# Performance work log

Measured on AMD Instinct MI355X. Metric: run time of the kernel, lower is better.

The kernel has to match this reference:

```python
import jax, jax.numpy as jnp
import numpy as np

B, M, D = 8, 8192, 1024   # batch, tokens, latent_dim
N, P = 128, 1             # num_experts, slots_per_expert
F = 4096                  # expert_dim


def setup_inputs() -> dict:
    key = jax.random.key(0)
    k_x, k_phi, k_w1, k_b1, k_w2, k_b2 = jax.random.split(key, 6)
    x = jax.random.normal(k_x, (B, M, D), dtype=jnp.float32)
    # phi initialized as randn(d, n, p) / sqrt(d) in the original
    phi = jax.random.normal(k_phi, (D, N, P), dtype=jnp.float32) / (D ** 0.5)
    # Single shared expert MLP (original aliases one nn.Sequential across all experts)
    W1 = jax.random.normal(k_w1, (D, F), dtype=jnp.float32) / (D ** 0.5)
    b1 = jax.random.normal(k_b1, (F,), dtype=jnp.float32) * 0.01
    W2 = jax.random.normal(k_w2, (F, D), dtype=jnp.float32) / (F ** 0.5)
    b2 = jax.random.normal(k_b2, (D,), dtype=jnp.float32) * 0.01
    return {"x": x, "phi": phi, "W1": W1, "b1": b1, "W2": W2, "b2": b2}


def reference(x, phi, W1, b1, W2, b2):
    # dispatch / combine logits: [b, m, n, p]
    logits = jnp.einsum('bmd,dnp->bmnp', x, phi)
    d = jax.nn.softmax(logits, axis=1)                      # softmax over tokens m
    b_, m_, n_, p_ = logits.shape
    c = jax.nn.softmax(logits.reshape(b_, m_, n_ * p_), axis=-1).reshape(b_, m_, n_, p_)
    # slot inputs: [b, n, p, d]
    x_i = jnp.einsum('bmd,bmnp->bnpd', x, d)
    # shared expert MLP (torch GELU default = exact erf)
    h = jax.nn.gelu(jnp.einsum('bnpd,df->bnpf', x_i, W1) + b1, approximate=False)
    y_i = jnp.einsum('bnpf,fd->bnpd', h, W2) + b2
    # combine: [b, m, d]
    y = jnp.einsum('bnpd,bmnp->bmd', y_i, c)
    return y
```

## Files before the change

### kernel.cpp

```cpp
#include <hip/hip_runtime.h>
#include <math.h>

#define Bq 8
#define Mq 8192
#define Dq 1024
#define Nq 128
#define Fq 4096

typedef __bf16 bf16x8 __attribute__((ext_vector_type(8)));
typedef float f32x4 __attribute__((ext_vector_type(4)));
union P4 { __bf16 h[4]; unsigned long long u; };
union H8 { int4 v; _Float16 h[8]; };
union B8 { int4 v; __bf16 h[8]; };

__device__ __forceinline__ int swz128(int row, int bcol) {
  return row * 128 + (bcol ^ ((row & 7) << 4));
}
__device__ __forceinline__ int swz256(int row, int bcol) {
  return row * 256 + (bcol ^ ((row & 7) << 4));
}

__global__ __launch_bounds__(256) void wconv(const float* __restrict__ src,
                                             unsigned long long* __restrict__ dst, long n4)
{
  long i = (long)blockIdx.x * 256 + threadIdx.x;
  if (i >= n4) return;
  float4 v = ((const float4*)src)[i];
  P4 p; p.h[0] = (__bf16)v.x; p.h[1] = (__bf16)v.y; p.h[2] = (__bf16)v.z; p.h[3] = (__bf16)v.w;
  dst[i] = p.u;
}

__global__ __launch_bounds__(256) void logits_mfma(
    const float* __restrict__ x, const float* __restrict__ phi,
    __bf16* __restrict__ eT, __bf16* __restrict__ cbuf)
{
  __shared__ __align__(16) char sA[16384];
  __shared__ __align__(16) char sP[16384];
  int mt = blockIdx.x, b = blockIdx.y;
  int m0 = mt * 128;
  int t = threadIdx.x;
  int col = t & 127, half = t >> 7;
  int arow = t >> 4, ac4 = t & 15;
  int w = t >> 6, l = t & 63, la = l & 15, lb = l >> 4;

  f32x4 zero = {0.f, 0.f, 0.f, 0.f};
  f32x4 acc[2][8];
  for (int i = 0; i < 2; ++i) for (int j = 0; j < 8; ++j) acc[i][j] = zero;

  for (int k0 = 0; k0 < Dq; k0 += 64) {
    #pragma unroll
    for (int i = 0; i < 8; ++i) {
      int row = arow + 16 * i;
      float4 v = *(const float4*)(x + ((long)b * Mq + m0 + row) * Dq + k0 + ac4 * 4);
      P4 p;
      p.h[0] = (__bf16)v.x; p.h[1] = (__bf16)v.y;
      p.h[2] = (__bf16)v.z; p.h[3] = (__bf16)v.w;
      *(unsigned long long*)(sA + swz128(row, 8 * ac4)) = p.u;
    }
    {
      const float* Pp = phi + (long)(k0 + half * 32) * Nq + col;
      #pragma unroll
      for (int i = 0; i < 32; i += 4) {
        float a0 = Pp[(i + 0) * Nq], a1 = Pp[(i + 1) * Nq];
        float a2 = Pp[(i + 2) * Nq], a3 = Pp[(i + 3) * Nq];
        P4 p;
        p.h[0] = (__bf16)a0; p.h[1] = (__bf16)a1;
        p.h[2] = (__bf16)a2; p.h[3] = (__bf16)a3;
        *(unsigned long long*)(sP + swz128(col, 2 * (half * 32 + i))) = p.u;
      }
    }
    __syncthreads();
    #pragma unroll
    for (int sub = 0; sub < 2; ++sub) {
      int mbyte = sub * 64 + lb * 16;
      bf16x8 af0 = *(const bf16x8*)(sA + swz128(w * 32 + la, mbyte));
      bf16x8 af1 = *(const bf16x8*)(sA + swz128(w * 32 + 16 + la, mbyte));
      bf16x8 bv[8];
      #pragma unroll
      for (int j = 0; j < 8; ++j)
        bv[j] = *(const bf16x8*)(sP + swz128(j * 16 + la, mbyte));
      #pragma unroll
      for (int j = 0; j < 8; ++j) {
        acc[0][j] = __builtin_amdgcn_mfma_f32_16x16x32_bf16(af0, bv[j], acc[0][j], 0, 0, 0);
        acc[1][j] = __builtin_amdgcn_mfma_f32_16x16x32_bf16(af1, bv[j], acc[1][j], 0, 0, 0);
      }
    }
    __syncthreads();
  }
  float inv[2][4];
  #pragma unroll
  for (int i = 0; i < 2; ++i)
    #pragma unroll
    for (int r = 0; r < 4; ++r) {
      float s = 0.f;
      #pragma unroll
      for (int j = 0; j < 8; ++j) s += __expf(acc[i][j][r]);
      s += __shfl_xor(s, 1); s += __shfl_xor(s, 2);
      s += __shfl_xor(s, 4); s += __shfl_xor(s, 8);
      inv[i][r] = 1.0f / s;
    }
  __bf16* Cb = cbuf + ((long)b * Mq + m0) * Nq;
  __bf16* Eb = eT + (long)b * Nq * Mq + m0;
  #pragma unroll
  for (int i = 0; i < 2; ++i)
    #pragma unroll
    for (int j = 0; j < 8; ++j) {
      P4 p;
      #pragma unroll
      for (int r = 0; r < 4; ++r) {
        int row = w * 32 + i * 16 + lb * 4 + r;
        float e = __expf(acc[i][j][r]);
        p.h[r] = (__bf16)e;
        Cb[(long)row * Nq + j * 16 + la] = (__bf16)(e * inv[i][r]);
      }
      *(unsigned long long*)(Eb + (long)(j * 16 + la) * Mq + w * 32 + i * 16 + lb * 4) = p.u;
    }
}

__global__ __launch_bounds__(256) void colsum_rows(const __bf16* __restrict__ eT,
                                                   float* __restrict__ cinv)
{
  __shared__ float red[4];
  int r = blockIdx.x;
  int t = threadIdx.x;
  const __bf16* p = eT + (long)r * Mq;
  float s = 0.f;
  #pragma unroll
  for (int k = 0; k < 4; ++k) {
    B8 v; v.v = *(const int4*)(p + t * 8 + k * 2048);
    #pragma unroll
    for (int e = 0; e < 8; ++e) s += (float)v.h[e];
  }
  #pragma unroll
  for (int off = 32; off >= 1; off >>= 1) s += __shfl_down(s, off);
  if ((t & 63) == 0) red[t >> 6] = s;
  __syncthreads();
  if (t == 0) cinv[r] = 1.0f / (red[0] + red[1] + red[2] + red[3]);
}

__global__ __launch_bounds__(256) void xi_mfma(
    const __bf16* __restrict__ eT, const float* __restrict__ x,
    _Float16* __restrict__ part)
{
  __shared__ __align__(16) char sD[16384];
  __shared__ __align__(16) char sX[8192];
  int dt = blockIdx.x, kc = blockIdx.y, b = blockIdx.z;
  int d0 = dt * 64;
  int t = threadIdx.x;
  int arow = t >> 1, ahalf = t & 1;
  const __bf16* Ep0 = eT + ((long)b * Nq + arow) * Mq + (long)kc * 1024 + ahalf * 32;
  int cd = t & 63, grp = t >> 6;
  const float* Xp0 = x + ((long)b * Mq + (long)kc * 1024 + grp * 16) * Dq + d0 + cd;
  int w = t >> 6, l = t & 63, la = l & 15, lb = l >> 4;

  f32x4 zero = {0.f, 0.f, 0.f, 0.f};
  f32x4 acc[2][4];
  for (int i = 0; i < 2; ++i) for (int j = 0; j < 4; ++j) acc[i][j] = zero;

  int4 ar[4];
  float br[16];
  #pragma unroll
  for (int q = 0; q < 4; ++q) ar[q] = *(const int4*)(Ep0 + q * 8);
  #pragma unroll
  for (int i = 0; i < 16; ++i) br[i] = Xp0[(long)i * Dq];
  #pragma unroll
  for (int q = 0; q < 4; ++q)
    *(int4*)(sD + swz128(arow, ahalf * 64 + q * 16)) = ar[q];
  #pragma unroll
  for (int q = 0; q < 4; ++q) {
    P4 p;
    p.h[0] = (__bf16)br[4 * q + 0]; p.h[1] = (__bf16)br[4 * q + 1];
    p.h[2] = (__bf16)br[4 * q + 2]; p.h[3] = (__bf16)br[4 * q + 3];
    *(unsigned long long*)(sX + swz128(cd, grp * 32 + q * 8)) = p.u;
  }

  for (int it = 0; it < 16; ++it) {
    __syncthreads();
    if (it < 15) {
      #pragma unroll
      for (int q = 0; q < 4; ++q)
        ar[q] = *(const int4*)(Ep0 + (it + 1) * 64 + q * 8);
      #pragma unroll
      for (int i = 0; i < 16; ++i)
        br[i] = Xp0[((long)(it + 1) * 64 + i) * Dq];
    }
    #pragma unroll
    for (int sub = 0; sub < 2; ++sub) {
      int mbyte = sub * 64 + lb * 16;
      bf16x8 af0 = *(const bf16x8*)(sD + swz128(w * 32 + la, mbyte));
      bf16x8 af1 = *(const bf16x8*)(sD + swz128(w * 32 + 16 + la, mbyte));
      bf16x8 bv[4];
      #pragma unroll
      for (int j = 0; j < 4; ++j)
        bv[j] = *(const bf16x8*)(sX + swz128(j * 16 + la, mbyte));
      #pragma unroll
      for (int j = 0; j < 4; ++j) {
        acc[0][j] = __builtin_amdgcn_mfma_f32_16x16x32_bf16(af0, bv[j], acc[0][j], 0, 0, 0);
        acc[1][j] = __builtin_amdgcn_mfma_f32_16x16x32_bf16(af1, bv[j], acc[1][j], 0, 0, 0);
      }
    }
    __syncthreads();
    if (it < 15) {
      #pragma unroll
      for (int q = 0; q < 4; ++q)
        *(int4*)(sD + swz128(arow, ahalf * 64 + q * 16)) = ar[q];
      #pragma unroll
      for (int q = 0; q < 4; ++q) {
        P4 p;
        p.h[0] = (__bf16)br[4 * q + 0]; p.h[1] = (__bf16)br[4 * q + 1];
        p.h[2] = (__bf16)br[4 * q + 2]; p.h[3] = (__bf16)br[4 * q + 3];
        *(unsigned long long*)(sX + swz128(cd, grp * 32 + q * 8)) = p.u;
      }
    }
  }
  _Float16* P = part + ((long)kc * Bq + b) * (long)Nq * Dq + d0;
  #pragma unroll
  for (int i = 0; i < 2; ++i)
    #pragma unroll
    for (int j = 0; j < 4; ++j)
      #pragma unroll
      for (int r = 0; r < 4; ++r)
        P[(long)(w * 32 + i * 16 + lb * 4 + r) * Dq + j * 16 + la] = (_Float16)acc[i][j][r];
}

__global__ __launch_bounds__(256) void xi_reduce(const _Float16* __restrict__ part,
    const float* __restrict__ cinv, __bf16* __restrict__ xib)
{
  long base = ((long)blockIdx.x * 256 + threadIdx.x) * 8;
  int row = (int)(base >> 10);
  float civ = cinv[row];
  float s[8] = {};
  #pragma unroll
  for (int k = 0; k < 8; ++k) {
    H8 v; v.v = *(const int4*)(part + (long)k * 1048576 + base);
    #pragma unroll
    for (int e = 0; e < 8; ++e) s[e] += (float)v.h[e];
  }
  B8 o;
  #pragma unroll
  for (int e = 0; e < 8; ++e) o.h[e] = (__bf16)(s[e] * civ);
  *(int4*)(xib + base) = o.v;
}

template<int EPI, typename OT>
__global__ __launch_bounds__(256) void gemm_bf16(const __bf16* __restrict__ A,
    const __bf16* __restrict__ Bw, const float* __restrict__ bias,
    OT* __restrict__ C, int lda, int ldb, int ldc, int kLen, long strideCz)
{
  __shared__ __align__(16) char sA[16384];
  __shared__ __align__(16) char sB[16384];
  int m0 = blockIdx.x * 128, n0 = blockIdx.y * 128;
  int kbase = blockIdx.z * kLen;
  C += (long)blockIdx.z * strideCz;
  int t = threadIdx.x;
  int col = t & 127, half = t >> 7;
  int w = t >> 6, l = t & 63, la = l & 15, lb = l >> 4;

  f32x4 zero = {0.f, 0.f, 0.f, 0.f};
  f32x4 acc[2][8];
  for (int i = 0; i < 2; ++i) for (int j = 0; j < 8; ++j) acc[i][j] = zero;

  for (int kt = 0; kt < kLen; kt += 64) {
    int kp = kbase + kt;
    #pragma unroll
    for (int s = 0; s < 4; ++s) {
      int idx = t + 256 * s;
      int row = idx >> 3, c8 = idx & 7;
      *(int4*)(sA + swz128(row, c8 * 16)) =
          *(const int4*)(A + (long)(m0 + row) * lda + kp + c8 * 8);
    }
    {
      const __bf16* Bp = Bw + (long)(kp + half * 32) * ldb + n0 + col;
      #pragma unroll
      for (int i = 0; i < 32; i += 4) {
        P4 p;
        p.h[0] = Bp[(long)(i + 0) * ldb]; p.h[1] = Bp[(long)(i + 1) * ldb];
        p.h[2] = Bp[(long)(i + 2) * ldb]; p.h[3] = Bp[(long)(i + 3) * ldb];
        *(unsigned long long*)(sB + swz128(col, 2 * (half * 32 + i))) = p.u;
      }
    }
    __syncthreads();
    #pragma unroll
    for (int sub = 0; sub < 2; ++sub) {
      int mbyte = sub * 64 + lb * 16;
      bf16x8 af0 = *(const bf16x8*)(sA + swz128(w * 32 + la, mbyte));
      bf16x8 af1 = *(const bf16x8*)(sA + swz128(w * 32 + 16 + la, mbyte));
      bf16x8 bv[8];
      #pragma unroll
      for (int j = 0; j < 8; ++j)
        bv[j] = *(const bf16x8*)(sB + swz128(j * 16 + la, mbyte));
      #pragma unroll
      for (int j = 0; j < 8; ++j) {
        acc[0][j] = __builtin_amdgcn_mfma_f32_16x16x32_bf16(af0, bv[j], acc[0][j], 0, 0, 0);
        acc[1][j] = __builtin_amdgcn_mfma_f32_16x16x32_bf16(af1, bv[j], acc[1][j], 0, 0, 0);
      }
    }
    __syncthreads();
  }
  #pragma unroll
  for (int i = 0; i < 2; ++i)
    #pragma unroll
    for (int j = 0; j < 8; ++j)
      #pragma unroll
      for (int r = 0; r < 4; ++r) {
        int row = m0 + w * 32 + i * 16 + lb * 4 + r;
        int colg = n0 + j * 16 + la;
        float v = acc[i][j][r];
        if (EPI == 2) {
          v += bias[colg];
          v = 0.5f * v * (1.0f + erff(v * 0.70710678118654752f));
        }
        C[(long)row * ldc + colg] = (OT)v;
      }
}

__global__ __launch_bounds__(256) void g2_reduce(const float* __restrict__ part,
    const float* __restrict__ b2, __bf16* __restrict__ yiT)
{
  long idx = (long)blockIdx.x * 256 + threadIdx.x;
  int row = (int)(idx >> 10);
  int d = (int)(idx & 1023);
  float s = part[idx] + part[idx + 1048576] + part[idx + 2097152] + part[idx + 3145728] + b2[d];
  int b = row >> 7, n = row & 127;
  yiT[((long)b * Dq + d) * Nq + n] = (__bf16)s;
}

__global__ __launch_bounds__(256) void combine_mfma(const __bf16* __restrict__ cbuf,
    const __bf16* __restrict__ yiT, float* __restrict__ y)
{
  __shared__ __align__(16) char sC[32768];
  __shared__ __align__(16) char sY[32768];
  int mt = blockIdx.x, dt = blockIdx.y, b = blockIdx.z;
  int m0 = mt * 128, d0 = dt * 128;
  int t = threadIdx.x;
  #pragma unroll
  for (int s = 0; s < 8; ++s) {
    int idx = t + 256 * s;
    int row = idx >> 4, c16 = idx & 15;
    *(int4*)(sC + swz256(row, c16 * 16)) =
        *(const int4*)(cbuf + ((long)b * Mq + m0 + row) * Nq + c16 * 8);
    *(int4*)(sY + swz256(row, c16 * 16)) =
        *(const int4*)(yiT + ((long)b * Dq + d0 + row) * Nq + c16 * 8);
  }
  __syncthreads();
  int w = t >> 6, l = t & 63, la = l & 15, lb = l >> 4;
  f32x4 zero = {0.f, 0.f, 0.f, 0.f};
  f32x4 acc[2][8];
  for (int i = 0; i < 2; ++i) for (int j = 0; j < 8; ++j) acc[i][j] = zero;
  #pragma unroll
  for (int sub = 0; sub < 4; ++sub) {
    int mbyte = sub * 64 + lb * 16;
    bf16x8 af0 = *(const bf16x8*)(sC + swz256(w * 32 + la, mbyte));
    bf16x8 af1 = *(const bf16x8*)(sC + swz256(w * 32 + 16 + la, mbyte));
    bf16x8 bv[8];
    #pragma unroll
    for (int j = 0; j < 8; ++j)
      bv[j] = *(const bf16x8*)(sY + swz256(j * 16 + la, mbyte));
    #pragma unroll
    for (int j = 0; j < 8; ++j) {
      acc[0][j] = __builtin_amdgcn_mfma_f32_16x16x32_bf16(af0, bv[j], acc[0][j], 0, 0, 0);
      acc[1][j] = __builtin_amdgcn_mfma_f32_16x16x32_bf16(af1, bv[j], acc[1][j], 0, 0, 0);
    }
  }
  float* Y = y + ((long)b * Mq + m0) * Dq + d0;
  #pragma unroll
  for (int i = 0; i < 2; ++i)
    #pragma unroll
    for (int j = 0; j < 8; ++j)
      #pragma unroll
      for (int r = 0; r < 4; ++r)
        Y[(long)(w * 32 + i * 16 + lb * 4 + r) * Dq + j * 16 + la] = acc[i][j][r];
}

extern "C" void kernel_launch(void* const* d_in, const int* in_sizes, int n_in,
                              void* d_out, int out_size, void* d_ws, size_t ws_size,
                              hipStream_t stream) {
  const float* x   = (const float*)d_in[0];
  const float* phi = (const float*)d_in[1];
  const float* W1  = (const float*)d_in[2];
  const float* b1  = (const float*)d_in[3];
  const float* W2  = (const float*)d_in[4];
  const float* b2  = (const float*)d_in[5];
  float* y = (float*)d_out;

  char* W = (char*)d_ws;
  __bf16*   cbuf   = (__bf16*)W;
  __bf16*   eT     = (__bf16*)(W + 16777216);
  __bf16*   h      = eT;
  _Float16* part   = (_Float16*)(W + 33554432);
  float*    g2part = (float*)(W + 33554432);
  __bf16*   W1b    = (__bf16*)(W + 50331648);
  __bf16*   W2b    = (__bf16*)(W + 58720256);
  __bf16*   xib    = (__bf16*)(W + 67108864);
  __bf16*   yiT    = (__bf16*)(W + 69206016);
  float*    cinv   = (float*)(W + 71303168);

  wconv<<<4096, 256, 0, stream>>>(W1, (unsigned long long*)W1b, 1048576);
  wconv<<<4096, 256, 0, stream>>>(W2, (unsigned long long*)W2b, 1048576);
  logits_mfma<<<dim3(Mq / 128, Bq), 256, 0, stream>>>(x, phi, eT, cbuf);
  colsum_rows<<<Bq * Nq, 256, 0, stream>>>(eT, cinv);
  xi_mfma<<<dim3(Dq / 64, 8, Bq), 256, 0, stream>>>(eT, x, part);
  xi_reduce<<<512, 256, 0, stream>>>(part, cinv, xib);
  gemm_bf16<2, __bf16><<<dim3(8, 32, 1), 256, 0, stream>>>(
      xib, W1b, b1, h, Dq, Fq, Fq, 1024, 0L);
  gemm_bf16<0, float><<<dim3(8, 8, 4), 256, 0, stream>>>(
      h, W2b, nullptr, g2part, Fq, Dq, Dq, 1024, 1048576L);
  g2_reduce<<<4096, 256, 0, stream>>>(g2part, b2, yiT);
  combine_mfma<<<dim3(Mq / 128, Dq / 128, Bq), 256, 0, stream>>>(cbuf, yiT, y);
}
```

Before: 440.0 us.

## Widen xi_mfma d-tile, vectorize x loads, and remap block order for L2 locality

The x_i GEMM kernel now covers 128 d-columns per block instead of 64. That halves the number of blocks re-reading the dispatch weights, and each thread loads x as float4 rows instead of scalar strided loads, at the cost of scalar bf16 transposed writes into shared memory. Both xi_mfma and combine_mfma switch to a 1D grid with a remapped block index, so neighbouring blocks share inputs and are spread across XCDs, which should improve L2 reuse. The wider tile doubles accumulator registers and grows shared memory, which may lower occupancy.

```diff
diff --git a/kernel.cpp b/kernel.cpp
--- a/kernel.cpp
+++ b/kernel.cpp
@@ -143,81 +143,73 @@
     _Float16* __restrict__ part)
 {
   __shared__ __align__(16) char sD[16384];
-  __shared__ __align__(16) char sX[8192];
-  int dt = blockIdx.x, kc = blockIdx.y, b = blockIdx.z;
-  int d0 = dt * 64;
+  __shared__ __align__(16) char sX[16384];
+  int lin = blockIdx.x;
+  int wk = (lin & 7) * 64 + (lin >> 3);
+  int dts = wk & 7, kc = (wk >> 3) & 7, b = wk >> 6;
+  int d0 = dts * 128;
   int t = threadIdx.x;
+  int w = t >> 6, l = t & 63, la = l & 15, lb = l >> 4;
   int arow = t >> 1, ahalf = t & 1;
-  const __bf16* Ep0 = eT + ((long)b * Nq + arow) * Mq + (long)kc * 1024 + ahalf * 32;
-  int cd = t & 63, grp = t >> 6;
-  const float* Xp0 = x + ((long)b * Mq + (long)kc * 1024 + grp * 16) * Dq + d0 + cd;
-  int w = t >> 6, l = t & 63, la = l & 15, lb = l >> 4;
+  const __bf16* Ep0 = eT + ((long)b * Nq + arow) * Mq + kc * 1024 + ahalf * 32;
+  int bm = w * 2 + (l >> 5), bd = (l & 31) * 4;
+  const float* Xp0 = x + ((long)b * Mq + kc * 1024 + bm) * Dq + d0 + bd;
 
   f32x4 zero = {0.f, 0.f, 0.f, 0.f};
-  f32x4 acc[2][4];
-  for (int i = 0; i < 2; ++i) for (int j = 0; j < 4; ++j) acc[i][j] = zero;
+  f32x4 acc[2][8];
+  for (int i = 0; i < 2; ++i) for (int j = 0; j < 8; ++j) acc[i][j] = zero;
 
   int4 ar[4];
-  float br[16];
+  float br[8][4];
   #pragma unroll
   for (int q = 0; q < 4; ++q) ar[q] = *(const int4*)(Ep0 + q * 8);
   #pragma unroll
-  for (int i = 0; i < 16; ++i) br[i] = Xp0[(long)i * Dq];
-  #pragma unroll
-  for (int q = 0; q < 4; ++q)
-    *(int4*)(sD + swz128(arow, ahalf * 64 + q * 16)) = ar[q];
-  #pragma unroll
-  for (int q = 0; q < 4; ++q) {
-    P4 p;
-    p.h[0] = (__bf16)br[4 * q + 0]; p.h[1] = (__bf16)br[4 * q + 1];
-    p.h[2] = (__bf16)br[4 * q + 2]; p.h[3] = (__bf16)br[4 * q + 3];
-    *(unsigned long long*)(sX + swz128(cd, grp * 32 + q * 8)) = p.u;
-  }
+  for (int k = 0; k < 8; ++k) *(float4*)br[k] = *(const float4*)(Xp0 + (long)k * 8 * Dq);
+  #pragma unroll
+  for (int q = 0; q < 4; ++q) *(int4*)(sD + swz128(arow, ahalf * 64 + q * 16)) = ar[q];
+  #pragma unroll
+  for (int k = 0; k < 8; ++k)
+    #pragma unroll
+    for (int q = 0; q < 4; ++q)
+      *(__bf16*)(sX + swz128(bd + q, 2 * (k * 8 + bm))) = (__bf16)br[k][q];
 
   for (int it = 0; it < 16; ++it) {
     __syncthreads();
     if (it < 15) {
       #pragma unroll
-      for (int q = 0; q < 4; ++q)
-        ar[q] = *(const int4*)(Ep0 + (it + 1) * 64 + q * 8);
-      #pragma unroll
-      for (int i = 0; i < 16; ++i)
-        br[i] = Xp0[((long)(it + 1) * 64 + i) * Dq];
+      for (int q = 0; q < 4; ++q) ar[q] = *(const int4*)(Ep0 + (it + 1) * 64 + q * 8);
+      #pragma unroll
+      for (int k = 0; k < 8; ++k)
+        *(float4*)br[k] = *(const float4*)(Xp0 + ((long)(it + 1) * 64 + k * 8) * Dq);
     }
     #pragma unroll
     for (int sub = 0; sub < 2; ++sub) {
       int mbyte = sub * 64 + lb * 16;
       bf16x8 af0 = *(const bf16x8*)(sD + swz128(w * 32 + la, mbyte));
       bf16x8 af1 = *(const bf16x8*)(sD + swz128(w * 32 + 16 + la, mbyte));
-      bf16x8 bv[4];
-      #pragma unroll
-      for (int j = 0; j < 4; ++j)
-        bv[j] = *(const bf16x8*)(sX + swz128(j * 16 + la, mbyte));
-      #pragma unroll
-      for (int j = 0; j < 4; ++j) {
-        acc[0][j] = __builtin_amdgcn_mfma_f32_16x16x32_bf16(af0, bv[j], acc[0][j], 0, 0, 0);
-        acc[1][j] = __builtin_amdgcn_mfma_f32_16x16x32_bf16(af1, bv[j], acc[1][j], 0, 0, 0);
+      #pragma unroll
+      for (int j = 0; j < 8; ++j) {
+        bf16x8 bv = *(const bf16x8*)(sX + swz128(j * 16 + la, mbyte));
+        acc[0][j] = __builtin_amdgcn_mfma_f32_16x16x32_bf16(af0, bv, acc[0][j], 0, 0, 0);
+        acc[1][j] = __builtin_amdgcn_mfma_f32_16x16x32_bf16(af1, bv, acc[1][j], 0, 0, 0);
       }
     }
     __syncthreads();
     if (it < 15) {
       #pragma unroll
-      for (int q = 0; q < 4; ++q)
-        *(int4*)(sD + swz128(arow, ahalf * 64 + q * 16)) = ar[q];
-      #pragma unroll
-      for (int q = 0; q < 4; ++q) {
-        P4 p;
-        p.h[0] = (__bf16)br[4 * q + 0]; p.h[1] = (__bf16)br[4 * q + 1];
-        p.h[2] = (__bf16)br[4 * q + 2]; p.h[3] = (__bf16)br[4 * q + 3];
-        *(unsigned long long*)(sX + swz128(cd, grp * 32 + q * 8)) = p.u;
-      }
+      for (int q = 0; q < 4; ++q) *(int4*)(sD + swz128(arow, ahalf * 64 + q * 16)) = ar[q];
+      #pragma unroll
+      for (int k = 0; k < 8; ++k)
+        #pragma unroll
+        for (int q = 0; q < 4; ++q)
+          *(__bf16*)(sX + swz128(bd + q, 2 * (k * 8 + bm))) = (__bf16)br[k][q];
     }
   }
   _Float16* P = part + ((long)kc * Bq + b) * (long)Nq * Dq + d0;
   #pragma unroll
   for (int i = 0; i < 2; ++i)
     #pragma unroll
-    for (int j = 0; j < 4; ++j)
+    for (int j = 0; j < 8; ++j)
       #pragma unroll
       for (int r = 0; r < 4; ++r)
         P[(long)(w * 32 + i * 16 + lb * 4 + r) * Dq + j * 16 + la] = (_Float16)acc[i][j][r];
@@ -330,7 +322,9 @@
 {
   __shared__ __align__(16) char sC[32768];
   __shared__ __align__(16) char sY[32768];
-  int mt = blockIdx.x, dt = blockIdx.y, b = blockIdx.z;
+  int lin = blockIdx.x;
+  int wk = (lin & 7) * 512 + (lin >> 3);
+  int dt = wk & 7, mt = (wk >> 3) & 63, b = wk >> 9;
   int m0 = mt * 128, d0 = dt * 128;
   int t = threadIdx.x;
   #pragma unroll
@@ -399,12 +393,12 @@
   wconv<<<4096, 256, 0, stream>>>(W2, (unsigned long long*)W2b, 1048576);
   logits_mfma<<<dim3(Mq / 128, Bq), 256, 0, stream>>>(x, phi, eT, cbuf);
   colsum_rows<<<Bq * Nq, 256, 0, stream>>>(eT, cinv);
-  xi_mfma<<<dim3(Dq / 64, 8, Bq), 256, 0, stream>>>(eT, x, part);
+  xi_mfma<<<512, 256, 0, stream>>>(eT, x, part);
   xi_reduce<<<512, 256, 0, stream>>>(part, cinv, xib);
   gemm_bf16<2, __bf16><<<dim3(8, 32, 1), 256, 0, stream>>>(
       xib, W1b, b1, h, Dq, Fq, Fq, 1024, 0L);
   gemm_bf16<0, float><<<dim3(8, 8, 4), 256, 0, stream>>>(
       h, W2b, nullptr, g2part, Fq, Dq, Dq, 1024, 1048576L);
   g2_reduce<<<4096, 256, 0, stream>>>(g2part, b2, yiT);
-  combine_mfma<<<dim3(Mq / 128, Dq / 128, Bq), 256, 0, stream>>>(cbuf, yiT, y);
-}
+  combine_mfma<<<4096, 256, 0, stream>>>(cbuf, yiT, y);
+}
```

Measured after the change: 377.3 us. -14.2%, faster.
